# Performance work log

Hardware: AMD Instinct MI355X
Metric: run time of the kernel (lower is better)

## Reference

```python
import jax, jax.numpy as jnp
import numpy as np

HIDDEN = 4096
N_EXPERTS = 128
TOP_K = 8
N_GROUP = 8
TOPK_GROUP = 4
ROUTED_SCALE = 1.0
NORM_TOPK = True
T = 32768


def setup_inputs() -> dict:
    key = jax.random.key(0)
    k1, k2, k3 = jax.random.split(key, 3)
    hidden_states = jax.random.normal(k1, (T, HIDDEN), dtype=jnp.float32)
    weight = jax.random.normal(k2, (N_EXPERTS, HIDDEN), dtype=jnp.float32) * 0.02
    e_score_correction_bias = jax.random.normal(k3, (N_EXPERTS,), dtype=jnp.float32) * 0.1
    return {"hidden_states": hidden_states, "weight": weight,
            "e_score_correction_bias": e_score_correction_bias}


def reference(hidden_states, weight, e_score_correction_bias):
    # GLM4-MoE top-k router: linear -> sigmoid -> bias-corrected grouped top-k
    x = hidden_states.reshape(-1, HIDDEN)
    router_logits = jnp.einsum('th,eh->te', x, weight)          # [T, E]
    scores = jax.nn.sigmoid(router_logits)                      # [T, E]
    scores_for_choice = scores + e_score_correction_bias[None, :]

    per_group = N_EXPERTS // N_GROUP
    g = scores_for_choice.reshape(-1, N_GROUP, per_group)       # [T, G, E/G]
    # group score = sum of top-2 expert scores within each group
    group_scores = jax.lax.top_k(g, 2)[0].sum(axis=-1)          # [T, G]
    group_idx = jax.lax.top_k(group_scores, TOPK_GROUP)[1]      # [T, topk_group]
    group_mask = jax.nn.one_hot(group_idx, N_GROUP, dtype=scores.dtype).sum(axis=1)  # [T, G]
    score_mask = jnp.repeat(group_mask, per_group, axis=-1)     # [T, E]
    masked_scores = jnp.where(score_mask > 0, scores_for_choice, 0.0)

    topk_indices = jax.lax.top_k(masked_scores, TOP_K)[1]       # [T, top_k]
    topk_weights = jnp.take_along_axis(scores, topk_indices, axis=1)  # gather raw (un-biased) scores
    if NORM_TOPK:
        denom = topk_weights.sum(axis=-1, keepdims=True) + 1e-20
        topk_weights = topk_weights / denom
    topk_weights = topk_weights * ROUTED_SCALE
    return topk_indices, topk_weights
```

## Files before the change

kernel.cpp:

```cpp
#include <hip/hip_runtime.h>
#include <math.h>

#define T_TOKENS 32768
#define HIDDEN   4096
#define NEXP     128
#define TM       64
#define BK       32
#define NSTAGE   (HIDDEN / BK)

#define A_PLANE_SH    2048
#define A_BUF_SH      (2 * A_PLANE_SH)
#define B_BASE_SH     (2 * A_BUF_SH)
#define B_PLANE_SH    4096
#define B_BUF_SH      (2 * B_PLANE_SH)
#define LDS_SHORTS    (B_BASE_SH + 2 * B_BUF_SH)
#define B_BASE_BYTES  (B_BASE_SH * 2)
#define B_BUF_BYTES   (B_BUF_SH * 2)
#define SC_STRIDE     129
#define B_CHUNK_BYTES B_BUF_BYTES
#define WS_BYTES ((size_t)NSTAGE * B_CHUNK_BYTES)

typedef _Float16 f16x8 __attribute__((ext_vector_type(8)));
typedef _Float16 f16x4 __attribute__((ext_vector_type(4)));
typedef float f32x4  __attribute__((ext_vector_type(4)));

__device__ __forceinline__ void split2(float x, _Float16& h0, _Float16& h1) {
    _Float16 a = (_Float16)x;
    float af = (float)a;
    if (__builtin_fabsf(af) < 6.103515625e-05f) { a = (_Float16)0.0f; af = 0.0f; }
    h0 = a;
    h1 = (_Float16)((x - af) * 4096.0f);
}

__global__ __launch_bounds__(256) void presplit_w(
    const float* __restrict__ w, _Float16* __restrict__ ws16)
{
    const int g = blockIdx.x * 256 + threadIdx.x;
    const int l = g & 63;
    const int t = (g >> 6) & 7;
    const int s = g >> 9;
    const int e  = t * 16 + (l & 15);
    const int kb = s * BK + ((l >> 4) & 3) * 8;
    const float* src = w + (size_t)e * HIDDEN + kb;
    float4 v0 = *(const float4*)(src);
    float4 v1 = *(const float4*)(src + 4);
    float vv[8] = {v0.x, v0.y, v0.z, v0.w, v1.x, v1.y, v1.z, v1.w};
    _Float16 h0[8], h1[8];
#pragma unroll
    for (int j = 0; j < 8; ++j) split2(vv[j], h0[j], h1[j]);
    _Float16* dst = ws16 + (size_t)s * 8192 + (t * 64 + l) * 8;
    *(f16x8*)(dst)        = (f16x8){h0[0],h0[1],h0[2],h0[3],h0[4],h0[5],h0[6],h0[7]};
    *(f16x8*)(dst + 4096) = (f16x8){h1[0],h1[1],h1[2],h1[3],h1[4],h1[5],h1[6],h1[7]};
}

__global__ __launch_bounds__(512, 4) void glm4_router_mfma(
    const float* __restrict__ x, const _Float16* __restrict__ wsplit,
    const float* __restrict__ bias, float* __restrict__ out)
{
    __shared__ __align__(16) _Float16 lds[LDS_SHORTS];

    const int tid  = threadIdx.x;
    const int wid  = tid >> 6;
    const int lane = tid & 63;
    const int rt_base = (wid & 1) * 2;
    const int ct_base = (wid >> 1) * 2;
    const int tok_base = blockIdx.x * TM;

    const int al = (tid >> 1) & 63;
    const int at = tid >> 7;
    const int arow = at * 16 + (al & 15);
    const int akoff = ((al >> 4) & 3) * 8 + (tid & 1) * 4;
    const float* xsrc = x + (size_t)(tok_base + arow) * HIDDEN + akoff;
    const int awr = tid * 4;

    f32x4 mainA[2][2];
    f32x4 corr[2][2];
    double accd[2][2][4];
#pragma unroll
    for (int r = 0; r < 2; ++r)
#pragma unroll
        for (int c = 0; c < 2; ++c) {
            mainA[r][c] = (f32x4){0.f, 0.f, 0.f, 0.f};
            corr[r][c]  = (f32x4){0.f, 0.f, 0.f, 0.f};
#pragma unroll
            for (int v = 0; v < 4; ++v) accd[r][c][v] = 0.0;
        }

#define GLDS_B(S, BUF) do {                                                    \
    const char* gsrc_ = (const char*)wsplit + (size_t)(S) * B_CHUNK_BYTES + tid * 16; \
    char* ldst_ = (char*)lds + B_BASE_BYTES + (BUF) * B_BUF_BYTES + tid * 16;  \
    __builtin_amdgcn_global_load_lds(                                          \
        (const __attribute__((address_space(1))) unsigned*)(gsrc_),            \
        (__attribute__((address_space(3))) unsigned*)(ldst_), 16, 0, 0);       \
    __builtin_amdgcn_global_load_lds(                                          \
        (const __attribute__((address_space(1))) unsigned*)(gsrc_ + 8192),     \
        (__attribute__((address_space(3))) unsigned*)(ldst_ + 8192), 16, 0, 0);\
} while (0)

#define SPLIT_A(XV, BUF) do {                                                  \
    _Float16 h0_[4], h1_[4];                                                   \
    split2((XV).x, h0_[0], h1_[0]);                                            \
    split2((XV).y, h0_[1], h1_[1]);                                            \
    split2((XV).z, h0_[2], h1_[2]);                                            \
    split2((XV).w, h0_[3], h1_[3]);                                            \
    _Float16* ab_ = &lds[(BUF) * A_BUF_SH + awr];                              \
    *(f16x4*)(ab_)              = (f16x4){h0_[0], h0_[1], h0_[2], h0_[3]};     \
    *(f16x4*)(ab_ + A_PLANE_SH) = (f16x4){h1_[0], h1_[1], h1_[2], h1_[3]};     \
} while (0)

#define MFMA_COL(C, B0_, B1_) do {                                             \
    _Pragma("unroll")                                                          \
    for (int r = 0; r < 2; ++r) {                                              \
        mainA[r][C] = __builtin_amdgcn_mfma_f32_16x16x32_f16(Af0[r], B0_, mainA[r][C], 0, 0, 0); \
        corr[r][C]  = __builtin_amdgcn_mfma_f32_16x16x32_f16(Af0[r], B1_, corr[r][C], 0, 0, 0);  \
        corr[r][C]  = __builtin_amdgcn_mfma_f32_16x16x32_f16(Af1[r], B0_, corr[r][C], 0, 0, 0);  \
    }                                                                          \
} while (0)

#define BODY(S, BUF, XC, XL) do {                                              \
    GLDS_B((S) + 1, (BUF) ^ 1);                                                \
    {                                                                          \
        int s2_ = (S) + 2; if (s2_ > NSTAGE - 1) s2_ = NSTAGE - 1;             \
        XL = *(const float4*)(xsrc + (size_t)s2_ * BK);                        \
    }                                                                          \
    f16x8 Af0[2], Af1[2];                                                      \
    _Pragma("unroll")                                                          \
    for (int r = 0; r < 2; ++r) {                                              \
        Af0[r] = *(const f16x8*)(&lds[(BUF) * A_BUF_SH                         \
                                      + ((rt_base + r) * 64 + lane) * 8]);     \
        Af1[r] = *(const f16x8*)(&lds[(BUF) * A_BUF_SH + A_PLANE_SH            \
                                      + ((rt_base + r) * 64 + lane) * 8]);     \
    }                                                                          \
    {                                                                          \
        f16x8 B0_ = *(const f16x8*)(&lds[B_BASE_SH + (BUF) * B_BUF_SH          \
                          + ((ct_base + 0) * 64 + lane) * 8]);                 \
        f16x8 B1_ = *(const f16x8*)(&lds[B_BASE_SH + (BUF) * B_BUF_SH          \
                          + B_PLANE_SH + ((ct_base + 0) * 64 + lane) * 8]);    \
        __builtin_amdgcn_s_setprio(1);                                         \
        MFMA_COL(0, B0_, B1_);                                                 \
        __builtin_amdgcn_s_setprio(0);                                         \
    }                                                                          \
    SPLIT_A(XC, (BUF) ^ 1);         \
    {                                                                          \
        f16x8 B0_ = *(const f16x8*)(&lds[B_BASE_SH + (BUF) * B_BUF_SH          \
                          + ((ct_base + 1) * 64 + lane) * 8]);                 \
        f16x8 B1_ = *(const f16x8*)(&lds[B_BASE_SH + (BUF) * B_BUF_SH          \
                          + B_PLANE_SH + ((ct_base + 1) * 64 + lane) * 8]);    \
        __builtin_amdgcn_s_setprio(1);                                         \
        MFMA_COL(1, B0_, B1_);                                                 \
        __builtin_amdgcn_s_setprio(0);                                         \
    }                                                                          \
    if (((S) & 3) == 3) {                                                      \
        _Pragma("unroll")                                                      \
        for (int r = 0; r < 2; ++r)                                            \
            _Pragma("unroll")                                                  \
            for (int c = 0; c < 2; ++c) {                                      \
                _Pragma("unroll")                                              \
                for (int v = 0; v < 4; ++v)                                    \
                    accd[r][c][v] += (double)mainA[r][c][v]                    \
                                   + (double)corr[r][c][v] * (1.0 / 4096.0);   \
                mainA[r][c] = (f32x4){0.f, 0.f, 0.f, 0.f};                     \
                corr[r][c]  = (f32x4){0.f, 0.f, 0.f, 0.f};                     \
            }                                                                  \
    }                                                                          \
    __syncthreads();       \
} while (0)

    float4 xA, xB;
    {
        float4 x0v = *(const float4*)(xsrc);
        GLDS_B(0, 0);
        xA = *(const float4*)(xsrc + BK);
        SPLIT_A(x0v, 0);
    }
    __syncthreads();

    for (int s = 0; s < NSTAGE - 2; s += 2) {
        BODY(s, 0, xA, xB);
        BODY(s + 1, 1, xB, xA);
    }
    BODY(NSTAGE - 2, 0, xA, xB);

    {
        f16x8 Af0[2], Af1[2];
#pragma unroll
        for (int r = 0; r < 2; ++r) {
            Af0[r] = *(const f16x8*)(&lds[1 * A_BUF_SH
                                          + ((rt_base + r) * 64 + lane) * 8]);
            Af1[r] = *(const f16x8*)(&lds[1 * A_BUF_SH + A_PLANE_SH
                                          + ((rt_base + r) * 64 + lane) * 8]);
        }
#pragma unroll
        for (int c = 0; c < 2; ++c) {
            f16x8 B0_ = *(const f16x8*)(&lds[B_BASE_SH + 1 * B_BUF_SH
                              + ((ct_base + c) * 64 + lane) * 8]);
            f16x8 B1_ = *(const f16x8*)(&lds[B_BASE_SH + 1 * B_BUF_SH
                              + B_PLANE_SH + ((ct_base + c) * 64 + lane) * 8]);
#pragma unroll
            for (int r = 0; r < 2; ++r) {
                mainA[r][c] = __builtin_amdgcn_mfma_f32_16x16x32_f16(Af0[r], B0_, mainA[r][c], 0, 0, 0);
                corr[r][c]  = __builtin_amdgcn_mfma_f32_16x16x32_f16(Af0[r], B1_, corr[r][c], 0, 0, 0);
                corr[r][c]  = __builtin_amdgcn_mfma_f32_16x16x32_f16(Af1[r], B0_, corr[r][c], 0, 0, 0);
            }
        }
#pragma unroll
        for (int r = 0; r < 2; ++r)
#pragma unroll
            for (int c = 0; c < 2; ++c)
#pragma unroll
                for (int v = 0; v < 4; ++v)
                    accd[r][c][v] += (double)mainA[r][c][v]
                                   + (double)corr[r][c][v] * (1.0 / 4096.0);
    }

    __syncthreads();
    float* sc = (float*)lds;
#pragma unroll
    for (int r = 0; r < 2; ++r)
#pragma unroll
        for (int c = 0; c < 2; ++c) {
#pragma unroll
            for (int v = 0; v < 4; ++v) {
                const int tokl = (rt_base + r) * 16 + (lane >> 4) * 4 + v;
                const int e    = (ct_base + c) * 16 + (lane & 15);
                const float lg = (float)accd[r][c][v];
                const float sg = (float)(1.0 / (1.0 + exp(-(double)lg)));
                sc[tokl * SC_STRIDE + e] = sg + bias[e];
            }
        }
    __syncthreads();

    if (tid < TM) {
        const float* scp = sc + tid * SC_STRIDE;

        float gsc[8];
#pragma unroll
        for (int g = 0; g < 8; ++g) {
            float m1 = -1e30f, m2 = -1e30f;
#pragma unroll
            for (int j = 0; j < 16; ++j) {
                const float v = scp[g * 16 + j];
                if (v > m1) { m2 = m1; m1 = v; }
                else if (v > m2) { m2 = v; }
            }
            gsc[g] = m1 + m2;
        }

        unsigned gmask = 0;
#pragma unroll
        for (int p = 0; p < 4; ++p) {
            float best = -1e30f; int bi = 0;
#pragma unroll
            for (int g = 0; g < 8; ++g) {
                const bool taken = (gmask >> g) & 1u;
                if (!taken && gsc[g] > best) { best = gsc[g]; bi = g; }
            }
            gmask |= 1u << bi;
        }

        unsigned long long chosen0 = 0ull, chosen1 = 0ull;
        int   idxs[8];
        float wts[8];
#pragma unroll
        for (int p = 0; p < 8; ++p) {
            float best = -1e30f; int bi = 0;
            for (int e = 0; e < NEXP; ++e) {
                const bool sel = (gmask >> (e >> 4)) & 1u;
                const float v = sel ? scp[e] : 0.0f;
                const bool ch = (e < 64) ? ((chosen0 >> e) & 1ull)
                                         : ((chosen1 >> (e - 64)) & 1ull);
                if (!ch && v > best) { best = v; bi = e; }
            }
            if (bi < 64) chosen0 |= 1ull << bi; else chosen1 |= 1ull << (bi - 64);
            idxs[p] = bi;
            wts[p] = scp[bi] - bias[bi];
        }

        float denom = 0.0f;
#pragma unroll
        for (int p = 0; p < 8; ++p) denom += wts[p];
        denom += 1e-20f;

        const size_t row = (size_t)(tok_base + tid) * 8;
        float* outI = out;
        float* outW = out + (size_t)T_TOKENS * 8;
#pragma unroll
        for (int p = 0; p < 8; ++p) {
            outI[row + p] = (float)idxs[p];
            outW[row + p] = wts[p] / denom;
        }
    }
}

extern "C" void kernel_launch(void* const* d_in, const int* in_sizes, int n_in,
                              void* d_out, int out_size, void* d_ws, size_t ws_size,
                              hipStream_t stream) {
    const float* x    = (const float*)d_in[0];
    const float* w    = (const float*)d_in[1];
    const float* bias = (const float*)d_in[2];
    float* out = (float*)d_out;
    _Float16* ws16 = (_Float16*)d_ws;

    presplit_w<<<dim3(NSTAGE * 8 * 64 / 256), 256, 0, stream>>>(w, ws16);
    glm4_router_mfma<<<dim3(T_TOKENS / TM), 512, 0, stream>>>(x, ws16, bias, out);
}
```

Baseline: 229.1 us.

## Enlarge token tile to 128 and widen per-wave expert columns

```diff
diff --git a/kernel.cpp b/kernel.cpp
--- a/kernel.cpp
+++ b/kernel.cpp
@@ -4,24 +4,23 @@
 #define T_TOKENS 32768
 #define HIDDEN   4096
 #define NEXP     128
-#define TM       64
+#define TM       128
 #define BK       32
 #define NSTAGE   (HIDDEN / BK)
 
-#define A_PLANE_SH    2048
-#define A_BUF_SH      (2 * A_PLANE_SH)
-#define B_BASE_SH     (2 * A_BUF_SH)
-#define B_PLANE_SH    4096
-#define B_BUF_SH      (2 * B_PLANE_SH)
-#define LDS_SHORTS    (B_BASE_SH + 2 * B_BUF_SH)
-#define B_BASE_BYTES  (B_BASE_SH * 2)
-#define B_BUF_BYTES   (B_BUF_SH * 2)
+#define A_PLANE_EL    4096
+#define A_BUF_EL      (2 * A_PLANE_EL)
+#define B_BASE_EL     (2 * A_BUF_EL)
+#define B_PLANE_EL    4096
+#define B_BUF_EL      (2 * B_PLANE_EL)
+#define LDS_ELEMS     33024
+#define B_BASE_BYTES  (B_BASE_EL * 2)
+#define B_BUF_BYTES   (B_BUF_EL * 2)
 #define SC_STRIDE     129
 #define B_CHUNK_BYTES B_BUF_BYTES
 #define WS_BYTES ((size_t)NSTAGE * B_CHUNK_BYTES)
 
 typedef _Float16 f16x8 __attribute__((ext_vector_type(8)));
-typedef _Float16 f16x4 __attribute__((ext_vector_type(4)));
 typedef float f32x4  __attribute__((ext_vector_type(4)));
 
 __device__ __forceinline__ void split2(float x, _Float16& h0, _Float16& h1) {
@@ -53,33 +52,31 @@
     *(f16x8*)(dst + 4096) = (f16x8){h1[0],h1[1],h1[2],h1[3],h1[4],h1[5],h1[6],h1[7]};
 }
 
-__global__ __launch_bounds__(512, 4) void glm4_router_mfma(
+__global__ __launch_bounds__(512, 2) void glm4_router_mfma(
     const float* __restrict__ x, const _Float16* __restrict__ wsplit,
     const float* __restrict__ bias, float* __restrict__ out)
 {
-    __shared__ __align__(16) _Float16 lds[LDS_SHORTS];
+    __shared__ __align__(16) _Float16 lds[LDS_ELEMS];
 
     const int tid  = threadIdx.x;
     const int wid  = tid >> 6;
     const int lane = tid & 63;
-    const int rt_base = (wid & 1) * 2;
-    const int ct_base = (wid >> 1) * 2;
+    const int rt_base = (wid & 3) * 2;
+    const int ct_base = (wid >> 2) * 4;
     const int tok_base = blockIdx.x * TM;
 
-    const int al = (tid >> 1) & 63;
-    const int at = tid >> 7;
-    const int arow = at * 16 + (al & 15);
-    const int akoff = ((al >> 4) & 3) * 8 + (tid & 1) * 4;
+    const int arow = ((tid >> 6) & 7) * 16 + (tid & 15);
+    const int akoff = ((tid >> 4) & 3) * 8;
     const float* xsrc = x + (size_t)(tok_base + arow) * HIDDEN + akoff;
-    const int awr = tid * 4;
-
-    f32x4 mainA[2][2];
-    f32x4 corr[2][2];
-    double accd[2][2][4];
+    const int awr = tid * 8;
+
+    f32x4 mainA[2][4];
+    f32x4 corr[2][4];
+    double accd[2][4][4];
 #pragma unroll
     for (int r = 0; r < 2; ++r)
 #pragma unroll
-        for (int c = 0; c < 2; ++c) {
+        for (int c = 0; c < 4; ++c) {
             mainA[r][c] = (f32x4){0.f, 0.f, 0.f, 0.f};
             corr[r][c]  = (f32x4){0.f, 0.f, 0.f, 0.f};
 #pragma unroll
@@ -97,15 +94,17 @@
         (__attribute__((address_space(3))) unsigned*)(ldst_ + 8192), 16, 0, 0);\
 } while (0)
 
-#define SPLIT_A(XV, BUF) do {                                                  \
-    _Float16 h0_[4], h1_[4];                                                   \
-    split2((XV).x, h0_[0], h1_[0]);                                            \
-    split2((XV).y, h0_[1], h1_[1]);                                            \
-    split2((XV).z, h0_[2], h1_[2]);                                            \
-    split2((XV).w, h0_[3], h1_[3]);                                            \
-    _Float16* ab_ = &lds[(BUF) * A_BUF_SH + awr];                              \
-    *(f16x4*)(ab_)              = (f16x4){h0_[0], h0_[1], h0_[2], h0_[3]};     \
-    *(f16x4*)(ab_ + A_PLANE_SH) = (f16x4){h1_[0], h1_[1], h1_[2], h1_[3]};     \
+#define SPLIT_A(XV0, XV1, BUF) do {                                            \
+    float vv_[8] = {(XV0).x, (XV0).y, (XV0).z, (XV0).w,                        \
+                    (XV1).x, (XV1).y, (XV1).z, (XV1).w};                       \
+    _Float16 h0_[8], h1_[8];                                                   \
+    _Pragma("unroll")                                                          \
+    for (int j = 0; j < 8; ++j) split2(vv_[j], h0_[j], h1_[j]);                \
+    _Float16* ab_ = &lds[(BUF) * A_BUF_EL + awr];                              \
+    *(f16x8*)(ab_) = (f16x8){h0_[0],h0_[1],h0_[2],h0_[3],                      \
+                             h0_[4],h0_[5],h0_[6],h0_[7]};                     \
+    *(f16x8*)(ab_ + A_PLANE_EL) = (f16x8){h1_[0],h1_[1],h1_[2],h1_[3],         \
+                                          h1_[4],h1_[5],h1_[6],h1_[7]};        \
 } while (0)
 
 #define MFMA_COL(C, B0_, B1_) do {                                             \
@@ -117,44 +116,49 @@
     }                                                                          \
 } while (0)
 
-#define BODY(S, BUF, XC, XL) do {                                              \
+#define BCOL(C, BUF, B0_, B1_)                                                 \
+    f16x8 B0_ = *(const f16x8*)(&lds[B_BASE_EL + (BUF) * B_BUF_EL              \
+                      + ((ct_base + (C)) * 64 + lane) * 8]);                   \
+    f16x8 B1_ = *(const f16x8*)(&lds[B_BASE_EL + (BUF) * B_BUF_EL              \
+                      + B_PLANE_EL + ((ct_base + (C)) * 64 + lane) * 8]);
+
+#define BODY(S, BUF, XC0, XC1, XL0, XL1) do {                                  \
     GLDS_B((S) + 1, (BUF) ^ 1);                                                \
     {                                                                          \
         int s2_ = (S) + 2; if (s2_ > NSTAGE - 1) s2_ = NSTAGE - 1;             \
-        XL = *(const float4*)(xsrc + (size_t)s2_ * BK);                        \
+        XL0 = *(const float4*)(xsrc + (size_t)s2_ * BK);                       \
+        XL1 = *(const float4*)(xsrc + (size_t)s2_ * BK + 4);                   \
     }                                                                          \
     f16x8 Af0[2], Af1[2];                                                      \
     _Pragma("unroll")                                                          \
     for (int r = 0; r < 2; ++r) {                                              \
-        Af0[r] = *(const f16x8*)(&lds[(BUF) * A_BUF_SH                         \
+        Af0[r] = *(const f16x8*)(&lds[(BUF) * A_BUF_EL                         \
                                       + ((rt_base + r) * 64 + lane) * 8]);     \
-        Af1[r] = *(const f16x8*)(&lds[(BUF) * A_BUF_SH + A_PLANE_SH            \
+        Af1[r] = *(const f16x8*)(&lds[(BUF) * A_BUF_EL + A_PLANE_EL            \
                                       + ((rt_base + r) * 64 + lane) * 8]);     \
     }                                                                          \
     {                                                                          \
-        f16x8 B0_ = *(const f16x8*)(&lds[B_BASE_SH + (BUF) * B_BUF_SH          \
-                          + ((ct_base + 0) * 64 + lane) * 8]);                 \
-        f16x8 B1_ = *(const f16x8*)(&lds[B_BASE_SH + (BUF) * B_BUF_SH          \
-                          + B_PLANE_SH + ((ct_base + 0) * 64 + lane) * 8]);    \
+        BCOL(0, BUF, Bc00, Bc01);                                              \
+        BCOL(1, BUF, Bc10, Bc11);                                              \
         __builtin_amdgcn_s_setprio(1);                                         \
-        MFMA_COL(0, B0_, B1_);                                                 \
+        MFMA_COL(0, Bc00, Bc01);                                               \
+        MFMA_COL(1, Bc10, Bc11);                                               \
         __builtin_amdgcn_s_setprio(0);                                         \
     }                                                                          \
-    SPLIT_A(XC, (BUF) ^ 1);         \
+    SPLIT_A(XC0, XC1, (BUF) ^ 1);   \
     {                                                                          \
-        f16x8 B0_ = *(const f16x8*)(&lds[B_BASE_SH + (BUF) * B_BUF_SH          \
-                          + ((ct_base + 1) * 64 + lane) * 8]);                 \
-        f16x8 B1_ = *(const f16x8*)(&lds[B_BASE_SH + (BUF) * B_BUF_SH          \
-                          + B_PLANE_SH + ((ct_base + 1) * 64 + lane) * 8]);    \
+        BCOL(2, BUF, Bc20, Bc21);                                              \
+        BCOL(3, BUF, Bc30, Bc31);                                              \
         __builtin_amdgcn_s_setprio(1);                                         \
-        MFMA_COL(1, B0_, B1_);                                                 \
+        MFMA_COL(2, Bc20, Bc21);                                               \
+        MFMA_COL(3, Bc30, Bc31);                                               \
         __builtin_amdgcn_s_setprio(0);                                         \
     }                                                                          \
     if (((S) & 3) == 3) {                                                      \
         _Pragma("unroll")                                                      \
         for (int r = 0; r < 2; ++r)                                            \
             _Pragma("unroll")                                                  \
-            for (int c = 0; c < 2; ++c) {                                      \
+            for (int c = 0; c < 4; ++c) {                                      \
                 _Pragma("unroll")                                              \
                 for (int v = 0; v < 4; ++v)                                    \
                     accd[r][c][v] += (double)mainA[r][c][v]                    \
@@ -166,36 +170,38 @@
     __syncthreads();       \
 } while (0)
 
-    float4 xA, xB;
+    float4 xA0, xA1, xB0, xB1;
     {
-        float4 x0v = *(const float4*)(xsrc);
+        float4 x00 = *(const float4*)(xsrc);
+        float4 x01 = *(const float4*)(xsrc + 4);
         GLDS_B(0, 0);
-        xA = *(const float4*)(xsrc + BK);
-        SPLIT_A(x0v, 0);
+        xA0 = *(const float4*)(xsrc + BK);
+        xA1 = *(const float4*)(xsrc + BK + 4);
+        SPLIT_A(x00, x01, 0);
     }
     __syncthreads();
 
     for (int s = 0; s < NSTAGE - 2; s += 2) {
-        BODY(s, 0, xA, xB);
-        BODY(s + 1, 1, xB, xA);
+        BODY(s, 0, xA0, xA1, xB0, xB1);
+        BODY(s + 1, 1, xB0, xB1, xA0, xA1);
     }
-    BODY(NSTAGE - 2, 0, xA, xB);
+    BODY(NSTAGE - 2, 0, xA0, xA1, xB0, xB1);
 
     {
         f16x8 Af0[2], Af1[2];
 #pragma unroll
         for (int r = 0; r < 2; ++r) {
-            Af0[r] = *(const f16x8*)(&lds[1 * A_BUF_SH
+            Af0[r] = *(const f16x8*)(&lds[1 * A_BUF_EL
                                           + ((rt_base + r) * 64 + lane) * 8]);
-            Af1[r] = *(const f16x8*)(&lds[1 * A_BUF_SH + A_PLANE_SH
+            Af1[r] = *(const f16x8*)(&lds[1 * A_BUF_EL + A_PLANE_EL
                                           + ((rt_base + r) * 64 + lane) * 8]);
         }
 #pragma unroll
-        for (int c = 0; c < 2; ++c) {
-            f16x8 B0_ = *(const f16x8*)(&lds[B_BASE_SH + 1 * B_BUF_SH
+        for (int c = 0; c < 4; ++c) {
+            f16x8 B0_ = *(const f16x8*)(&lds[B_BASE_EL + 1 * B_BUF_EL
                               + ((ct_base + c) * 64 + lane) * 8]);
-            f16x8 B1_ = *(const f16x8*)(&lds[B_BASE_SH + 1 * B_BUF_SH
-                              + B_PLANE_SH + ((ct_base + c) * 64 + lane) * 8]);
+            f16x8 B1_ = *(const f16x8*)(&lds[B_BASE_EL + 1 * B_BUF_EL
+                              + B_PLANE_EL + ((ct_base + c) * 64 + lane) * 8]);
 #pragma unroll
             for (int r = 0; r < 2; ++r) {
                 mainA[r][c] = __builtin_amdgcn_mfma_f32_16x16x32_f16(Af0[r], B0_, mainA[r][c], 0, 0, 0);
@@ -206,7 +212,7 @@
 #pragma unroll
         for (int r = 0; r < 2; ++r)
 #pragma unroll
-            for (int c = 0; c < 2; ++c)
+            for (int c = 0; c < 4; ++c)
 #pragma unroll
                 for (int v = 0; v < 4; ++v)
                     accd[r][c][v] += (double)mainA[r][c][v]
@@ -218,7 +224,7 @@
 #pragma unroll
     for (int r = 0; r < 2; ++r)
 #pragma unroll
-        for (int c = 0; c < 2; ++c) {
+        for (int c = 0; c < 4; ++c) {
 #pragma unroll
             for (int v = 0; v < 4; ++v) {
                 const int tokl = (rt_base + r) * 16 + (lane >> 4) * 4 + v;
```

After: 253.6 us. 1.11x slower.
